# Kernel tuning notes

Hardware: AMD Instinct MI355X
Metric: run time of the kernel (lower is better)

## Reference

```python
import jax, jax.numpy as jnp
import numpy as np

BETA = 0.9
T = 16
THR = 1.0
SLOPE = 25.0  # snntorch surrogate.fast_sigmoid default slope


@jax.custom_vjp
def spike(x):
    # Heaviside forward, fast-sigmoid surrogate backward (snntorch fast_sigmoid)
    return (x > 0.0).astype(x.dtype)

def _spike_fwd(x):
    return spike(x), x

def _spike_bwd(x, g):
    return (g / (SLOPE * jnp.abs(x) + 1.0) ** 2,)

spike.defvjp(_spike_fwd, _spike_bwd)


def conv1d(x, w, b, pad):
    # x: (B, C_in, L), w: (C_out, C_in, K)
    y = jax.lax.conv_general_dilated(
        x, w, window_strides=(1,), padding=[(pad, pad)],
        dimension_numbers=("NCH", "OIH", "NCH"))
    return y + b[None, :, None]


def lif(cur, mem):
    # snntorch Leaky, reset_mechanism='subtract', threshold=1.0.
    # reset spike is computed from the PREVIOUS membrane and detached.
    reset = jax.lax.stop_gradient((mem > THR).astype(cur.dtype))
    mem = BETA * mem + cur - reset * THR
    spk = spike(mem - THR)
    return spk, mem


def setup_inputs() -> dict:
    key = jax.random.key(0)
    ks = jax.random.split(key, 14)

    def u(k, shape, fan_in):
        bound = 1.0 / np.sqrt(fan_in)
        return jax.random.uniform(k, shape, jnp.float32, -bound, bound)

    x = jax.random.normal(ks[0], (2048, 2, 128), dtype=jnp.float32)
    W1 = u(ks[1], (256, 2, 5), 2 * 5);    b1 = u(ks[2], (256,), 2 * 5)
    W2 = u(ks[3], (128, 256, 3), 256 * 3); b2 = u(ks[4], (128,), 256 * 3)
    W3 = u(ks[5], (64, 128, 3), 128 * 3);  b3 = u(ks[6], (64,), 128 * 3)
    W4 = u(ks[7], (2, 64, 3), 64 * 3);     b4 = u(ks[8], (2,), 64 * 3)
    fw1 = u(ks[9], (100, 256), 256);       fb1 = u(ks[10], (100,), 256)
    fw2 = u(ks[11], (40, 100), 100);       fb2 = u(ks[12], (40,), 100)
    return {"x": x, "W1": W1, "b1": b1, "W2": W2, "b2": b2,
            "W3": W3, "b3": b3, "W4": W4, "b4": b4,
            "fw1": fw1, "fb1": fb1, "fw2": fw2, "fb2": fb2}


def reference(x, W1, b1, W2, b2, W3, b3, W4, b4, fw1, fb1, fw2, fb2):
    B, _, L = x.shape
    f32 = x.dtype
    # conv1 input is constant across timesteps -> hoist (same math)
    cur1 = conv1d(x, W1, b1, 2)
    init = (jnp.zeros((B, 256, L), f32), jnp.zeros((B, 128, L), f32),
            jnp.zeros((B, 64, L), f32), jnp.zeros((B, 2, L), f32),
            jnp.zeros((B, 100), f32), jnp.zeros((B, 40), f32))

    def step(carry, _):
        m1, m2, m3, m4, m5, acc = carry
        s1, m1 = lif(cur1, m1)
        s2, m2 = lif(conv1d(s1, W2, b2, 1), m2)
        s3, m3 = lif(conv1d(s2, W3, b3, 1), m3)
        s4, m4 = lif(conv1d(s3, W4, b4, 1), m4)
        flat = s4.reshape(B, -1)                      # (B, 256)
        s5, m5 = lif(flat @ fw1.T + fb1, m5)
        acc = acc + s5 @ fw2.T + fb2
        return (m1, m2, m3, m4, m5, acc), None

    (_, _, _, _, _, acc), _ = jax.lax.scan(step, init, None, length=T)
    return acc / T
```

## Files before the change

kernel.cpp:

```cpp
#include <hip/hip_runtime.h>
#include <stdint.h>

#define BETA 0.9f

typedef unsigned short u16;
typedef unsigned char u8;
typedef signed char i8;
typedef int i32x4 __attribute__((ext_vector_type(4)));

__device__ __forceinline__ void async_copy16(const void* g, void* l) {
  __builtin_amdgcn_global_load_lds(
      (const __attribute__((address_space(1))) uint32_t*)g,
      (__attribute__((address_space(3))) uint32_t*)l, 16, 0, 0);
}

__global__ void prep_kernel(const float* __restrict__ W2, const float* __restrict__ W3,
                            const float* __restrict__ fw1, const float* __restrict__ fw2,
                            i8* __restrict__ A2c, i8* __restrict__ A3c,
                            float* __restrict__ fw1T, float* __restrict__ fw2T) {
  int o = blockIdx.x * 256 + threadIdx.x;
  if (o < 98304) {
    int tap = o >> 15, r = o & 32767, co = r >> 8, ci = r & 255;
    float w = W2[(co * 256 + ci) * 3 + tap];
    float d0 = __builtin_rintf(w * 0x1p11f);
    float r1 = w - d0 * 0x1p-11f;
    float d1 = __builtin_rintf(r1 * 0x1p18f);
    float r2 = r1 - d1 * 0x1p-18f;
    float d2 = __builtin_rintf(r2 * 0x1p25f);
    int cp = ci >> 6, cl = ci & 63;
    int ct = co >> 6, col = co & 63;
    int gs = ((cl >> 4) ^ ((col >> 1) & 3)) & 3;
    int pos = gs * 16 + (cl & 15);
    size_t base = ((size_t)((0 * 4 + cp) * 2 + ct) * 3 + tap) * 64 * 64 + col * 64 + pos;
    size_t pstride = (size_t)4 * 2 * 3 * 64 * 64;
    A2c[base] = (i8)(int)d0;
    A2c[pstride + base] = (i8)(int)d1;
    A2c[2 * pstride + base] = (i8)(int)d2;
  }
  int o2 = o - 98304;
  if (o2 >= 0 && o2 < 24576) {
    int tap = o2 >> 13, r = o2 & 8191, co = r >> 7, ci = r & 127;
    float w = W3[(co * 128 + ci) * 3 + tap];
    float d0 = __builtin_rintf(w * 0x1p11f);
    float r1 = w - d0 * 0x1p-11f;
    float d1 = __builtin_rintf(r1 * 0x1p18f);
    float r2 = r1 - d1 * 0x1p-18f;
    float d2 = __builtin_rintf(r2 * 0x1p25f);
    int cp = ci >> 6, cl = ci & 63;
    int gs = ((cl >> 4) ^ ((co >> 1) & 3)) & 3;
    int pos = gs * 16 + (cl & 15);
    size_t base = ((size_t)(0 * 2 + cp) * 3 + tap) * 64 * 64 + co * 64 + pos;
    size_t pstride = (size_t)2 * 3 * 64 * 64;
    A3c[base] = (i8)(int)d0;
    A3c[pstride + base] = (i8)(int)d1;
    A3c[2 * pstride + base] = (i8)(int)d2;
  }
  int o3 = o - (98304 + 24576);
  if (o3 >= 0 && o3 < 25600) {
    int f = o3 / 100, i = o3 % 100;
    fw1T[o3] = fw1[i * 256 + f];
  }
  int o4 = o - (98304 + 24576 + 25600);
  if (o4 >= 0 && o4 < 4000) {
    int i = o4 / 40, j = o4 % 40;
    fw2T[o4] = fw2[j * 100 + i];
  }
}

__global__ __launch_bounds__(256) void conv1_lif_kernel(
    const float* __restrict__ x, const float* __restrict__ W1,
    const float* __restrict__ b1, u8* __restrict__ SBT2) {
  __shared__ float xl[2][132];
  __shared__ u16 bl[8][128];
  int b = blockIdx.x, g = blockIdx.y;
  int tid = threadIdx.x;
  for (int i = tid; i < 264; i += 256) {
    int ci = i / 132, idx = i % 132, lg = idx - 2;
    xl[ci][idx] = (lg >= 0 && lg < 128) ? x[(b * 2 + ci) * 128 + lg] : 0.0f;
  }
  __syncthreads();
  int cosub = tid >> 5, tx = tid & 31;
  int co = g * 8 + cosub;
  float w[2][5];
#pragma unroll
  for (int ci = 0; ci < 2; ++ci)
#pragma unroll
    for (int k = 0; k < 5; ++k) w[ci][k] = W1[(co * 2 + ci) * 5 + k];
  float bias = b1[co];
  float cur[4];
#pragma unroll
  for (int j = 0; j < 4; ++j) {
    float acc = bias;
#pragma unroll
    for (int ci = 0; ci < 2; ++ci)
#pragma unroll
      for (int k = 0; k < 5; ++k) acc += w[ci][k] * xl[ci][4 * tx + j + k];
    cur[j] = acc;
  }
  float m[4] = {0.f, 0.f, 0.f, 0.f}, sp[4] = {0.f, 0.f, 0.f, 0.f};
  uint32_t bits[4] = {0u, 0u, 0u, 0u};
#pragma unroll
  for (int t = 0; t < 16; ++t) {
#pragma unroll
    for (int j = 0; j < 4; ++j) {
      m[j] = BETA * m[j] + cur[j] - sp[j];
      bool s = m[j] > 1.0f;
      bits[j] |= ((uint32_t)s) << t;
      sp[j] = s ? 1.0f : 0.0f;
    }
  }
#pragma unroll
  for (int j = 0; j < 4; ++j) bl[cosub][4 * tx + j] = (u16)bits[j];
  __syncthreads();
  if (tid < 128) {
    int l = tid;
    uint32_t wv[8];
#pragma unroll
    for (int j = 0; j < 8; ++j) wv[j] = bl[j][l];
    uint32_t ov[4];
#pragma unroll
    for (int k = 0; k < 4; ++k) {
      uint32_t v = 0;
#pragma unroll
      for (int tt = 0; tt < 4; ++tt) {
        int t = k * 4 + tt;
        uint32_t by = 0;
#pragma unroll
        for (int j = 0; j < 8; ++j) by |= ((wv[j] >> t) & 1u) << j;
        v |= by << (8 * tt);
      }
      ov[k] = v;
    }
    *(uint4*)(SBT2 + ((size_t)(b * 128 + l) * 32 + g) * 16) =
        make_uint4(ov[0], ov[1], ov[2], ov[3]);
  }
}

template <int CIN, int COUT, bool SBTOUT>
__global__ __launch_bounds__(256, 3) void conv_mfma_kernel(
    const u8* __restrict__ SBT, const i8* __restrict__ Agc,
    const float* __restrict__ bias, void* __restrict__ outp) {
  constexpr int NCP = CIN / 64;
  constexpr int LNCP = (NCP == 4) ? 2 : 1;
  constexpr int NVIRT = 3 * NCP;
  constexpr int NCT = COUT / 64;
  constexpr int MT = 2, NT = 8;
  constexpr int GB = CIN / 8;
  constexpr int ABYTES = 3 * 64 * 64;
  constexpr int AW = ABYTES / 4;
  constexpr int AISS = AW / 1024;
  __shared__ __align__(16) char lds[2 * ABYTES];
  __shared__ __align__(16) u8 Bs[18 * 16 * 80];
  __shared__ __align__(8) uint2 LUT[256];

  int b = blockIdx.x, lb = blockIdx.y * 16, ct = blockIdx.z;
  int tid = threadIdx.x, lane = tid & 63, wid = tid >> 6;
  int wx = wid & 1, wy = wid >> 1;
  int q = lane >> 4, xx = lane & 15;
  int mloc = wy * 32;
  int gs16 = ((q ^ ((xx >> 1) & 3)) & 3) * 16;

  {
    uint32_t by = tid;
    uint32_t lo = ((by & 0xFu) * 0x204081u) & 0x01010101u;
    uint32_t hi = (((by >> 4) & 0xFu) * 0x204081u) & 0x01010101u;
    LUT[tid] = make_uint2(lo, hi);
  }

  i32x4 acc[MT][NT];
#pragma unroll
  for (int mt = 0; mt < MT; ++mt)
#pragma unroll
    for (int nt = 0; nt < NT; ++nt) acc[mt][nt] = (i32x4){0, 0, 0, 0};

  auto mkbase = [&](int s, const u8*& ptr, bool& vf) {
    int row = s >> 5, gl = s & 7, tq = (s >> 3) & 3;
    int l_in = lb + row - 1;
    vf = ((unsigned)l_in < 128u);
    int l_c = vf ? l_in : 0;
    ptr = SBT + ((size_t)(b * 128 + l_c) * GB + gl) * 16 + tq * 4;
  };
  const u8 *sp0, *sp1, *sp2 = nullptr;
  bool f0, f1, f2 = false;
  mkbase(tid, sp0, f0);
  mkbase(tid + 256, sp1, f1);
  if (tid < 64) mkbase(tid + 512, sp2, f2);

  auto stage_write = [&](int s, uint32_t w4) {
    int row = s >> 5, gl = s & 7, tq = (s >> 3) & 3;
    u8* dst = Bs + (row * 16 + tq * 4) * 80 + gl * 8;
#pragma unroll
    for (int i = 0; i < 4; ++i)
      *(uint2*)(dst + i * 80) = LUT[(w4 >> (8 * i)) & 0xFFu];
  };

  auto ablock = [&](int v) -> size_t {
    int p = v >> LNCP, j = v & (NCP - 1);
    int cp = (p & 1) ? (NCP - 1 - j) : j;
    return ((size_t)(p * NCP + cp) * NCT + ct) * (size_t)ABYTES;
  };

  uint32_t w4a = f0 ? *(const uint32_t*)sp0 : 0u;
  uint32_t w4b = f1 ? *(const uint32_t*)sp1 : 0u;
  uint32_t w4c = (tid < 64 && f2) ? *(const uint32_t*)sp2 : 0u;
  {
    const char* gsrc = (const char*)Agc + (size_t)wid * AW + lane * 16 + ablock(0);
    char* ldst = lds + wid * AW;
#pragma unroll
    for (int i = 0; i < AISS; ++i) async_copy16(gsrc + i * 1024, ldst + i * 1024);
  }

  i32x4 Bf[10];
  for (int v = 0; v < NVIRT; ++v) {
    int p = v >> LNCP, j = v & (NCP - 1);
    bool stg = (v == 0) || (j != 0);
    __syncthreads();
    if (stg) {
      stage_write(tid, w4a);
      stage_write(tid + 256, w4b);
      if (tid < 64) stage_write(tid + 512, w4c);
      __syncthreads();
    }
    if (v + 1 < NVIRT) {
      const char* gsrc = (const char*)Agc + (size_t)wid * AW + lane * 16 + ablock(v + 1);
      char* ldst = lds + ((v + 1) & 1) * ABYTES + wid * AW;
#pragma unroll
      for (int i = 0; i < AISS; ++i) async_copy16(gsrc + i * 1024, ldst + i * 1024);
    }
    if (stg) {
      int jn = j + 1, pn = p;
      if (jn == NCP) { pn = p + 1; jn = 1; }
      if (pn < 3) {
        int cpn = (pn & 1) ? (NCP - 1 - jn) : jn;
        w4a = f0 ? *(const uint32_t*)(sp0 + cpn * 128) : 0u;
        w4b = f1 ? *(const uint32_t*)(sp1 + cpn * 128) : 0u;
        if (tid < 64) w4c = f2 ? *(const uint32_t*)(sp2 + cpn * 128) : 0u;
      }
#pragma unroll
      for (int u = 0; u < 10; ++u)
        Bf[u] = *(const i32x4*)(Bs + ((wx * 8 + u) * 16 + xx) * 80 + q * 16);
    }
    if (j == 0 && p > 0) {
#pragma unroll
      for (int mt = 0; mt < MT; ++mt)
#pragma unroll
        for (int nt = 0; nt < NT; ++nt) acc[mt][nt] = acc[mt][nt] << 7;
    }
    const i8* Asv = (const i8*)(lds + (v & 1) * ABYTES);
#pragma unroll
    for (int tap = 0; tap < 3; ++tap)
#pragma unroll
      for (int mt = 0; mt < MT; ++mt) {
        i32x4 Af = *(const i32x4*)(Asv + (tap * 64 + mloc + mt * 16 + xx) * 64 + gs16);
#pragma unroll
        for (int nt = 0; nt < NT; ++nt)
          acc[mt][nt] = __builtin_amdgcn_mfma_i32_16x16x64_i8(
              Af, Bf[nt + tap], acc[mt][nt], 0, 0, 0);
      }
  }
  __syncthreads();

  float* scr = (float*)(void*)lds + wid * 1216;
  u16* bl = (u16*)(lds + 19456);
#pragma unroll
  for (int mt = 0; mt < MT; ++mt) {
#pragma unroll
    for (int h = 0; h < 2; ++h) {
#pragma unroll
      for (int u2 = 0; u2 < 4; ++u2)
#pragma unroll
        for (int r = 0; r < 4; ++r)
          scr[(u2 * 16 + q * 4 + r) * 19 + xx] =
              (float)acc[mt][h * 4 + u2][r] * 0x1p-25f;
      __syncthreads();
      int col = mloc + mt * 16 + xx;
      float bc = bias[ct * 64 + col];
      const float* rowp = scr + (q * 16 + xx) * 19;
      float mm = 0.f, sp = 0.f;
      uint32_t bits = 0;
#pragma unroll
      for (int t = 0; t < 16; ++t) {
        float cur = rowp[t] + bc;
        mm = BETA * mm + cur - sp;
        bool s = mm > 1.0f;
        bits |= ((uint32_t)s) << t;
        sp = s ? 1.0f : 0.0f;
      }
      bl[col * 16 + wx * 8 + h * 4 + q] = (u16)bits;
      __syncthreads();
    }
  }

  if constexpr (SBTOUT) {
    constexpr int GBo = COUT / 8;
    if (tid < 128) {
      int g = tid & 7, ll = tid >> 3;
      uint32_t wv[8];
#pragma unroll
      for (int j2 = 0; j2 < 8; ++j2) wv[j2] = bl[(8 * g + j2) * 16 + ll];
      uint32_t ov[4];
#pragma unroll
      for (int k = 0; k < 4; ++k) {
        uint32_t v = 0;
#pragma unroll
        for (int tt = 0; tt < 4; ++tt) {
          int t = k * 4 + tt;
          uint32_t by = 0;
#pragma unroll
          for (int j2 = 0; j2 < 8; ++j2) by |= ((wv[j2] >> t) & 1u) << j2;
          v |= by << (8 * tt);
        }
        ov[k] = v;
      }
      *(uint4*)((u8*)outp + ((size_t)(b * 128 + lb + ll) * GBo + ct * 8 + g) * 16) =
          make_uint4(ov[0], ov[1], ov[2], ov[3]);
    }
  } else {
    if (tid < 128) {
      int col = tid >> 1, hf = tid & 1;
      uint4 v = *(const uint4*)(bl + col * 16 + hf * 8);
      *(uint4*)((u16*)outp + ((size_t)b * COUT + ct * 64 + col) * 128 + lb + hf * 8) = v;
    }
  }
}

__global__ __launch_bounds__(256) void head_kernel(
    const u16* __restrict__ s3bits, const float* __restrict__ W4,
    const float* __restrict__ b4, const float* __restrict__ fw1T,
    const float* __restrict__ fb1, const float* __restrict__ fw2T,
    const float* __restrict__ fb2, float* __restrict__ out) {
  __shared__ u16 s3l[64][130];
  __shared__ float W4l[384];
  __shared__ u16 flat4[256];
  __shared__ u16 s5b[100];
  int b = blockIdx.x, tid = threadIdx.x;

  for (int i = tid; i < 64 * 130; i += 256) {
    int ci = i / 130, idx = i % 130, lg = idx - 1;
    s3l[ci][idx] = (lg >= 0 && lg < 128) ? s3bits[((size_t)b * 64 + ci) * 128 + lg] : (u16)0;
  }
  for (int i = tid; i < 384; i += 256) W4l[i] = W4[i];
  __syncthreads();

  {
    int co = tid >> 7, l = tid & 127;
    float acc4[16];
#pragma unroll
    for (int t = 0; t < 16; ++t) acc4[t] = 0.f;
    for (int ci = 0; ci < 64; ++ci) {
#pragma unroll
      for (int k = 0; k < 3; ++k) {
        float wv = W4l[(co * 64 + ci) * 3 + k];
        uint32_t msk = s3l[ci][l + k];
#pragma unroll
        for (int t = 0; t < 16; ++t)
          acc4[t] = fmaf(wv, (float)((msk >> t) & 1u), acc4[t]);
      }
    }
    float bc = b4[co];
    float m = 0.f, sp = 0.f;
    uint32_t bits = 0;
#pragma unroll
    for (int t = 0; t < 16; ++t) {
      m = BETA * m + (acc4[t] + bc) - sp;
      bool s = m > 1.0f;
      bits |= ((uint32_t)s) << t;
      sp = s ? 1.0f : 0.0f;
    }
    flat4[tid] = (u16)bits;
  }
  __syncthreads();

  float* part5 = (float*)&s3l[0][0];
  float acc5[16];
#pragma unroll
  for (int t = 0; t < 16; ++t) acc5[t] = 0.f;
  int n5 = tid % 100, h5 = tid / 100;
  if (tid < 200) {
    const float* wp = fw1T + (h5 * 128) * 100 + n5;
    for (int f = 0; f < 128; ++f) {
      float wv = wp[f * 100];
      uint32_t msk = flat4[h5 * 128 + f];
#pragma unroll
      for (int t = 0; t < 16; ++t)
        acc5[t] = fmaf(wv, (float)((msk >> t) & 1u), acc5[t]);
    }
    if (h5 == 1) {
#pragma unroll
      for (int t = 0; t < 16; ++t) part5[n5 * 16 + t] = acc5[t];
    }
  }
  __syncthreads();
  if (tid < 100) {
    float bc = fb1[tid];
    float m = 0.f, sp = 0.f;
    uint32_t bits = 0;
#pragma unroll
    for (int t = 0; t < 16; ++t) {
      float cur = acc5[t] + part5[tid * 16 + t] + bc;
      m = BETA * m + cur - sp;
      bool s = m > 1.0f;
      bits |= ((uint32_t)s) << t;
      sp = s ? 1.0f : 0.0f;
    }
    s5b[tid] = (u16)bits;
  }
  __syncthreads();

  if (tid < 40) {
    float a = 0.f;
    for (int i = 0; i < 100; ++i) {
      float wv = fw2T[i * 40 + tid];
      a = fmaf(wv, (float)__popc((uint32_t)s5b[i]), a);
    }
    out[b * 40 + tid] = a * 0.0625f + fb2[tid];
  }
}

extern "C" void kernel_launch(void* const* d_in, const int* in_sizes, int n_in,
                              void* d_out, int out_size, void* d_ws, size_t ws_size,
                              hipStream_t stream) {
  const float* x   = (const float*)d_in[0];
  const float* W1  = (const float*)d_in[1];
  const float* b1  = (const float*)d_in[2];
  const float* W2  = (const float*)d_in[3];
  const float* b2  = (const float*)d_in[4];
  const float* W3  = (const float*)d_in[5];
  const float* b3  = (const float*)d_in[6];
  const float* W4  = (const float*)d_in[7];
  const float* b4  = (const float*)d_in[8];
  const float* fw1 = (const float*)d_in[9];
  const float* fb1 = (const float*)d_in[10];
  const float* fw2 = (const float*)d_in[11];
  const float* fb2 = (const float*)d_in[12];
  float* out = (float*)d_out;

  char* ws = (char*)d_ws;
  i8*    A2c  = (i8*)(ws);
  i8*    A3c  = (i8*)(ws + 294912);
  float* fw1T = (float*)(ws + 368640);
  float* fw2T = (float*)(ws + 471040);
  u8*    SBT2 = (u8*)(ws + 487424);
  u8*    SBT3 = (u8*)(ws + 487424 + 134217728);
  u16*   s3b  = (u16*)(ws + 487424 + 134217728 + 67108864);

  prep_kernel<<<dim3(596), dim3(256), 0, stream>>>(W2, W3, fw1, fw2, A2c, A3c, fw1T, fw2T);
  conv1_lif_kernel<<<dim3(2048, 32), dim3(256), 0, stream>>>(x, W1, b1, SBT2);
  conv_mfma_kernel<256, 128, true><<<dim3(2048, 8, 2), dim3(256), 0, stream>>>(SBT2, A2c, b2, SBT3);
  conv_mfma_kernel<128, 64, false><<<dim3(2048, 8, 1), dim3(256), 0, stream>>>(SBT3, A3c, b3, s3b);
  head_kernel<<<dim3(2048), dim3(256), 0, stream>>>(s3b, W4, b4, fw1T, fb1, fw2T, fb2, out);
}
```

Baseline: 1.850 ms.

## Reorganize spike bit layout so MFMA B operands load directly from global

Changes the packed spike-train layout to per-(position, timestep) channel bitmasks. conv1 now produces it with wave ballots across channels, replacing the LDS bit-transpose. The MFMA conv kernels read 16-bit channel masks straight from global memory into registers and expand them arithmetically, dropping the LDS B staging buffer, the LUT and one barrier per stage. This lowers LDS use and synchronisation, but brings more scattered small global loads and extra ALU work for expansion.

```diff
diff --git a/kernel.cpp b/kernel.cpp
--- a/kernel.cpp
+++ b/kernel.cpp
@@ -70,70 +70,52 @@
 __global__ __launch_bounds__(256) void conv1_lif_kernel(
     const float* __restrict__ x, const float* __restrict__ W1,
     const float* __restrict__ b1, u8* __restrict__ SBT2) {
-  __shared__ float xl[2][132];
-  __shared__ u16 bl[8][128];
-  int b = blockIdx.x, g = blockIdx.y;
-  int tid = threadIdx.x;
-  for (int i = tid; i < 264; i += 256) {
-    int ci = i / 132, idx = i % 132, lg = idx - 2;
+  __shared__ float xl[2][12];
+  int b = blockIdx.x, lb8 = blockIdx.y * 8;
+  int tid = threadIdx.x, lane = tid & 63, w = tid >> 6;
+  int co = w * 64 + lane;
+  if (tid < 24) {
+    int ci = tid / 12, idx = tid % 12, lg = lb8 + idx - 2;
     xl[ci][idx] = (lg >= 0 && lg < 128) ? x[(b * 2 + ci) * 128 + lg] : 0.0f;
   }
-  __syncthreads();
-  int cosub = tid >> 5, tx = tid & 31;
-  int co = g * 8 + cosub;
-  float w[2][5];
+  float wgt[2][5];
 #pragma unroll
   for (int ci = 0; ci < 2; ++ci)
 #pragma unroll
-    for (int k = 0; k < 5; ++k) w[ci][k] = W1[(co * 2 + ci) * 5 + k];
+    for (int k = 0; k < 5; ++k) wgt[ci][k] = W1[(co * 2 + ci) * 5 + k];
   float bias = b1[co];
-  float cur[4];
-#pragma unroll
-  for (int j = 0; j < 4; ++j) {
-    float acc = bias;
+  __syncthreads();
+  float cur[8];
+#pragma unroll
+  for (int j = 0; j < 8; ++j) {
+    float a = bias;
 #pragma unroll
     for (int ci = 0; ci < 2; ++ci)
 #pragma unroll
-      for (int k = 0; k < 5; ++k) acc += w[ci][k] * xl[ci][4 * tx + j + k];
-    cur[j] = acc;
-  }
-  float m[4] = {0.f, 0.f, 0.f, 0.f}, sp[4] = {0.f, 0.f, 0.f, 0.f};
-  uint32_t bits[4] = {0u, 0u, 0u, 0u};
-#pragma unroll
-  for (int t = 0; t < 16; ++t) {
-#pragma unroll
-    for (int j = 0; j < 4; ++j) {
-      m[j] = BETA * m[j] + cur[j] - sp[j];
-      bool s = m[j] > 1.0f;
-      bits[j] |= ((uint32_t)s) << t;
-      sp[j] = s ? 1.0f : 0.0f;
-    }
-  }
-#pragma unroll
-  for (int j = 0; j < 4; ++j) bl[cosub][4 * tx + j] = (u16)bits[j];
-  __syncthreads();
-  if (tid < 128) {
-    int l = tid;
-    uint32_t wv[8];
-#pragma unroll
-    for (int j = 0; j < 8; ++j) wv[j] = bl[j][l];
-    uint32_t ov[4];
-#pragma unroll
-    for (int k = 0; k < 4; ++k) {
-      uint32_t v = 0;
-#pragma unroll
-      for (int tt = 0; tt < 4; ++tt) {
-        int t = k * 4 + tt;
-        uint32_t by = 0;
-#pragma unroll
-        for (int j = 0; j < 8; ++j) by |= ((wv[j] >> t) & 1u) << j;
-        v |= by << (8 * tt);
-      }
-      ov[k] = v;
-    }
-    *(uint4*)(SBT2 + ((size_t)(b * 128 + l) * 32 + g) * 16) =
-        make_uint4(ov[0], ov[1], ov[2], ov[3]);
-  }
+      for (int k = 0; k < 5; ++k) a += wgt[ci][k] * xl[ci][j + k];
+    cur[j] = a;
+  }
+  unsigned long long st0 = 0ull, st1 = 0ull;
+#pragma unroll
+  for (int l = 0; l < 8; ++l) {
+    float m = 0.f, sp = 0.f;
+#pragma unroll
+    for (int t = 0; t < 16; ++t) {
+      m = BETA * m + cur[l] - sp;
+      bool s = m > 1.0f;
+      unsigned long long bal = __ballot(s);
+      int p = l * 16 + t;
+      if ((p & 63) == lane) {
+        if (p < 64) st0 = bal; else st1 = bal;
+      }
+      sp = s ? 1.0f : 0.0f;
+    }
+  }
+  int l0 = lane >> 4, t0 = lane & 15;
+  *(uint2*)(SBT2 + ((size_t)(b * 128 + lb8 + l0) * 16 + t0) * 32 + w * 8) =
+      *(uint2*)&st0;
+  *(uint2*)(SBT2 + ((size_t)(b * 128 + lb8 + 4 + l0) * 16 + t0) * 32 + w * 8) =
+      *(uint2*)&st1;
 }
 
 template <int CIN, int COUT, bool SBTOUT>
@@ -150,59 +132,48 @@
   constexpr int AW = ABYTES / 4;
   constexpr int AISS = AW / 1024;
   __shared__ __align__(16) char lds[2 * ABYTES];
-  __shared__ __align__(16) u8 Bs[18 * 16 * 80];
-  __shared__ __align__(8) uint2 LUT[256];
 
   int b = blockIdx.x, lb = blockIdx.y * 16, ct = blockIdx.z;
   int tid = threadIdx.x, lane = tid & 63, wid = tid >> 6;
   int wx = wid & 1, wy = wid >> 1;
   int q = lane >> 4, xx = lane & 15;
   int mloc = wy * 32;
+  int lw = lb + wx * 8;
   int gs16 = ((q ^ ((xx >> 1) & 3)) & 3) * 16;
 
-  {
-    uint32_t by = tid;
-    uint32_t lo = ((by & 0xFu) * 0x204081u) & 0x01010101u;
-    uint32_t hi = (((by >> 4) & 0xFu) * 0x204081u) & 0x01010101u;
-    LUT[tid] = make_uint2(lo, hi);
-  }
-
   i32x4 acc[MT][NT];
 #pragma unroll
   for (int mt = 0; mt < MT; ++mt)
 #pragma unroll
     for (int nt = 0; nt < NT; ++nt) acc[mt][nt] = (i32x4){0, 0, 0, 0};
 
-  auto mkbase = [&](int s, const u8*& ptr, bool& vf) {
-    int row = s >> 5, gl = s & 7, tq = (s >> 3) & 3;
-    int l_in = lb + row - 1;
-    vf = ((unsigned)l_in < 128u);
-    int l_c = vf ? l_in : 0;
-    ptr = SBT + ((size_t)(b * 128 + l_c) * GB + gl) * 16 + tq * 4;
+  auto load_byt = [&](int cp, uint32_t* dst) {
+#pragma unroll
+    for (int u = 0; u < 10; ++u) {
+      int l_in = lw + u - 1;
+      dst[u] = ((unsigned)l_in < 128u)
+                   ? (uint32_t)*(const u16*)(SBT +
+                         ((size_t)(b * 128 + l_in) * 16 + xx) * GB + cp * 8 + 2 * q)
+                   : 0u;
+    }
   };
-  const u8 *sp0, *sp1, *sp2 = nullptr;
-  bool f0, f1, f2 = false;
-  mkbase(tid, sp0, f0);
-  mkbase(tid + 256, sp1, f1);
-  if (tid < 64) mkbase(tid + 512, sp2, f2);
-
-  auto stage_write = [&](int s, uint32_t w4) {
-    int row = s >> 5, gl = s & 7, tq = (s >> 3) & 3;
-    u8* dst = Bs + (row * 16 + tq * 4) * 80 + gl * 8;
-#pragma unroll
-    for (int i = 0; i < 4; ++i)
-      *(uint2*)(dst + i * 80) = LUT[(w4 >> (8 * i)) & 0xFFu];
+  auto expand = [&](uint32_t y) -> i32x4 {
+    uint32_t b0 = y & 0xFFu, b1 = (y >> 8) & 0xFFu;
+    i32x4 r;
+    r.x = (int)(((b0 & 0xFu) * 0x204081u) & 0x01010101u);
+    r.y = (int)(((b0 >> 4) * 0x204081u) & 0x01010101u);
+    r.z = (int)(((b1 & 0xFu) * 0x204081u) & 0x01010101u);
+    r.w = (int)(((b1 >> 4) * 0x204081u) & 0x01010101u);
+    return r;
   };
-
   auto ablock = [&](int v) -> size_t {
     int p = v >> LNCP, j = v & (NCP - 1);
     int cp = (p & 1) ? (NCP - 1 - j) : j;
     return ((size_t)(p * NCP + cp) * NCT + ct) * (size_t)ABYTES;
   };
 
-  uint32_t w4a = f0 ? *(const uint32_t*)sp0 : 0u;
-  uint32_t w4b = f1 ? *(const uint32_t*)sp1 : 0u;
-  uint32_t w4c = (tid < 64 && f2) ? *(const uint32_t*)sp2 : 0u;
+  uint32_t byt[10];
+  load_byt(0, byt);
   {
     const char* gsrc = (const char*)Agc + (size_t)wid * AW + lane * 16 + ablock(0);
     char* ldst = lds + wid * AW;
@@ -215,12 +186,6 @@
     int p = v >> LNCP, j = v & (NCP - 1);
     bool stg = (v == 0) || (j != 0);
     __syncthreads();
-    if (stg) {
-      stage_write(tid, w4a);
-      stage_write(tid + 256, w4b);
-      if (tid < 64) stage_write(tid + 512, w4c);
-      __syncthreads();
-    }
     if (v + 1 < NVIRT) {
       const char* gsrc = (const char*)Agc + (size_t)wid * AW + lane * 16 + ablock(v + 1);
       char* ldst = lds + ((v + 1) & 1) * ABYTES + wid * AW;
@@ -228,17 +193,14 @@
       for (int i = 0; i < AISS; ++i) async_copy16(gsrc + i * 1024, ldst + i * 1024);
     }
     if (stg) {
+#pragma unroll
+      for (int u = 0; u < 10; ++u) Bf[u] = expand(byt[u]);
       int jn = j + 1, pn = p;
       if (jn == NCP) { pn = p + 1; jn = 1; }
       if (pn < 3) {
         int cpn = (pn & 1) ? (NCP - 1 - jn) : jn;
-        w4a = f0 ? *(const uint32_t*)(sp0 + cpn * 128) : 0u;
-        w4b = f1 ? *(const uint32_t*)(sp1 + cpn * 128) : 0u;
-        if (tid < 64) w4c = f2 ? *(const uint32_t*)(sp2 + cpn * 128) : 0u;
-      }
-#pragma unroll
-      for (int u = 0; u < 10; ++u)
-        Bf[u] = *(const i32x4*)(Bs + ((wx * 8 + u) * 16 + xx) * 80 + q * 16);
+        load_byt(cpn, byt);
+      }
     }
     if (j == 0 && p > 0) {
 #pragma unroll
@@ -261,7 +223,7 @@
   __syncthreads();
 
   float* scr = (float*)(void*)lds + wid * 1216;
-  u16* bl = (u16*)(lds + 19456);
+  u16* blx = (u16*)(lds + 19456);
 #pragma unroll
   for (int mt = 0; mt < MT; ++mt) {
 #pragma unroll
@@ -286,39 +248,37 @@
         bits |= ((uint32_t)s) << t;
         sp = s ? 1.0f : 0.0f;
       }
-      bl[col * 16 + wx * 8 + h * 4 + q] = (u16)bits;
+      int ll = wx * 8 + h * 4 + q;
+      if constexpr (SBTOUT) blx[ll * 64 + col] = (u16)bits;
+      else                  blx[col * 16 + ll] = (u16)bits;
       __syncthreads();
     }
   }
 
   if constexpr (SBTOUT) {
-    constexpr int GBo = COUT / 8;
-    if (tid < 128) {
-      int g = tid & 7, ll = tid >> 3;
-      uint32_t wv[8];
-#pragma unroll
-      for (int j2 = 0; j2 < 8; ++j2) wv[j2] = bl[(8 * g + j2) * 16 + ll];
-      uint32_t ov[4];
-#pragma unroll
-      for (int k = 0; k < 4; ++k) {
-        uint32_t v = 0;
-#pragma unroll
-        for (int tt = 0; tt < 4; ++tt) {
-          int t = k * 4 + tt;
-          uint32_t by = 0;
-#pragma unroll
-          for (int j2 = 0; j2 < 8; ++j2) by |= ((wv[j2] >> t) & 1u) << j2;
-          v |= by << (8 * tt);
-        }
-        ov[k] = v;
-      }
-      *(uint4*)((u8*)outp + ((size_t)(b * 128 + lb + ll) * GBo + ct * 8 + g) * 16) =
-          make_uint4(ov[0], ov[1], ov[2], ov[3]);
-    }
+    int l = tid >> 4, t = tid & 15;
+    uint4 rows[8];
+#pragma unroll
+    for (int r = 0; r < 8; ++r) rows[r] = *(const uint4*)(blx + l * 64 + r * 8);
+    uint32_t lo = 0, hi = 0;
+#pragma unroll
+    for (int g = 0; g < 8; ++g) {
+      uint32_t wv[4] = {rows[g].x, rows[g].y, rows[g].z, rows[g].w};
+      uint32_t by = 0;
+#pragma unroll
+      for (int j2 = 0; j2 < 8; ++j2) {
+        uint32_t h16 = (wv[j2 >> 1] >> (16 * (j2 & 1))) & 0xFFFFu;
+        by |= ((h16 >> t) & 1u) << j2;
+      }
+      if (g < 4) lo |= by << (8 * g);
+      else       hi |= by << (8 * (g - 4));
+    }
+    *(uint2*)((u8*)outp + ((size_t)(b * 128 + lb + l) * 16 + t) * 16 + ct * 8) =
+        make_uint2(lo, hi);
   } else {
     if (tid < 128) {
       int col = tid >> 1, hf = tid & 1;
-      uint4 v = *(const uint4*)(bl + col * 16 + hf * 8);
+      uint4 v = *(const uint4*)(blx + col * 16 + hf * 8);
       *(uint4*)((u16*)outp + ((size_t)b * COUT + ct * 64 + col) * 128 + lb + hf * 8) = v;
     }
   }
@@ -445,7 +405,7 @@
   u16*   s3b  = (u16*)(ws + 487424 + 134217728 + 67108864);
 
   prep_kernel<<<dim3(596), dim3(256), 0, stream>>>(W2, W3, fw1, fw2, A2c, A3c, fw1T, fw2T);
-  conv1_lif_kernel<<<dim3(2048, 32), dim3(256), 0, stream>>>(x, W1, b1, SBT2);
+  conv1_lif_kernel<<<dim3(2048, 16), dim3(256), 0, stream>>>(x, W1, b1, SBT2);
   conv_mfma_kernel<256, 128, true><<<dim3(2048, 8, 2), dim3(256), 0, stream>>>(SBT2, A2c, b2, SBT3);
   conv_mfma_kernel<128, 64, false><<<dim3(2048, 8, 1), dim3(256), 0, stream>>>(SBT3, A3c, b3, s3b);
   head_kernel<<<dim3(2048), dim3(256), 0, stream>>>(s3b, W4, b4, fw1T, fb1, fw2T, fb2, out);
```

Result: slower. 2.821 ms (+52.5%).
